# Performance work log

Hardware: AMD Instinct MI355X
Metric: run time of the kernel (lower is better)

## Reference

```python
import jax, jax.numpy as jnp
import numpy as np

HEADS = 8
DH = 160
LN_EPS = 1e-5


def _ln(x):
    m = jnp.mean(x, axis=-1, keepdims=True)
    v = jnp.var(x, axis=-1, keepdims=True)
    return (x - m) * jax.lax.rsqrt(v + LN_EPS)


def _adaln(x, table, w, b, t):
    # table[t]: [dim]; emb -> [2*dim]; chunk along dim 0 (scalar timestep)
    emb = jax.nn.silu(table[t]) @ w + b
    scale, shift = jnp.split(emb, 2)
    return _ln(x) * (1.0 + scale) + shift


def _attn(x, ctx, wq, wk, wv, wo, bo):
    B, S, _ = x.shape
    Sk = ctx.shape[1]
    q = (x @ wq).reshape(B, S, HEADS, DH).transpose(0, 2, 1, 3)    # [B,H,S,dh]
    k = (ctx @ wk).reshape(B, Sk, HEADS, DH).transpose(0, 2, 1, 3)
    v = (ctx @ wv).reshape(B, Sk, HEADS, DH).transpose(0, 2, 1, 3)
    scores = jnp.einsum('bhid,bhjd->bhij', q, k) * (DH ** -0.5)
    probs = jax.nn.softmax(scores, axis=-1)
    o = jnp.einsum('bhij,bhjd->bhid', probs, v)
    o = o.transpose(0, 2, 1, 3).reshape(B, S, HEADS * DH)
    return o @ wo + bo


def _ff(x, w1, b1, w2, b2):
    h, gate = jnp.split(x @ w1 + b1, 2, axis=-1)
    return (h * jax.nn.gelu(gate, approximate=False)) @ w2 + b2


def setup_inputs() -> dict:
    key = jax.random.key(0)
    ks = jax.random.split(key, 24)
    B, S, SC, DIM, CROSS, INNER = 2, 2048, 77, 1280, 768, 5120

    def w(k, shape, s=0.02):
        return jax.random.normal(k, shape, jnp.float32) * s

    return {
        'hidden_states': jax.random.normal(ks[0], (B, S, DIM), jnp.float32),
        'context': jax.random.normal(ks[1], (B, SC, CROSS), jnp.float32),
        'ada1_emb': w(ks[2], (1000, DIM)),
        'ada1_w': w(ks[3], (DIM, 2 * DIM)),
        'ada1_b': jnp.zeros((2 * DIM,), jnp.float32),
        'ada2_emb': w(ks[4], (1000, DIM)),
        'ada2_w': w(ks[5], (DIM, 2 * DIM)),
        'ada2_b': jnp.zeros((2 * DIM,), jnp.float32),
        'a1_wq': w(ks[6], (DIM, DIM)), 'a1_wk': w(ks[7], (DIM, DIM)),
        'a1_wv': w(ks[8], (DIM, DIM)), 'a1_wo': w(ks[9], (DIM, DIM)),
        'a1_bo': jnp.zeros((DIM,), jnp.float32),
        'a2_wq': w(ks[10], (DIM, DIM)), 'a2_wk': w(ks[11], (CROSS, DIM)),
        'a2_wv': w(ks[12], (CROSS, DIM)), 'a2_wo': w(ks[13], (DIM, DIM)),
        'a2_bo': jnp.zeros((DIM,), jnp.float32),
        'norm3_g': jnp.ones((DIM,), jnp.float32),
        'norm3_b': jnp.zeros((DIM,), jnp.float32),
        'ff_w1': w(ks[14], (DIM, 2 * INNER)),
        'ff_b1': jnp.zeros((2 * INNER,), jnp.float32),
        'ff_w2': w(ks[15], (INNER, DIM)),
        'ff_b2': jnp.zeros((DIM,), jnp.float32),
        'timestep': 500,
    }


def reference(hidden_states, context, ada1_emb, ada1_w, ada1_b, ada2_emb, ada2_w, ada2_b,
              a1_wq, a1_wk, a1_wv, a1_wo, a1_bo, a2_wq, a2_wk, a2_wv, a2_wo, a2_bo,
              norm3_g, norm3_b, ff_w1, ff_b1, ff_w2, ff_b2, timestep):
    x = hidden_states
    # self-attention with AdaLayerNorm
    h = _adaln(x, ada1_emb, ada1_w, ada1_b, timestep)
    x = x + _attn(h, h, a1_wq, a1_wk, a1_wv, a1_wo, a1_bo)
    # cross-attention with AdaLayerNorm
    h = _adaln(x, ada2_emb, ada2_w, ada2_b, timestep)
    x = x + _attn(h, context, a2_wq, a2_wk, a2_wv, a2_wo, a2_bo)
    # feed-forward with affine LayerNorm
    h = _ln(x) * norm3_g + norm3_b
    x = x + _ff(h, ff_w1, ff_b1, ff_w2, ff_b2)
    return x
```

## Files before the change

### kernel.cpp

```cpp
#include <hip/hip_runtime.h>

typedef __attribute__((ext_vector_type(8))) unsigned short ushort8;
typedef __attribute__((ext_vector_type(4))) float f32x4;
typedef __attribute__((ext_vector_type(8))) __bf16 bf16x8;
typedef unsigned short u16;

__device__ inline unsigned short f2bf(float f) {
  unsigned u = __float_as_uint(f);
  unsigned r = (u + 0x7fffu + ((u >> 16) & 1u)) >> 16;
  return (unsigned short)r;
}
__device__ inline float bf2f(unsigned short h) {
  return __uint_as_float(((unsigned)h) << 16);
}

__device__ __forceinline__ void gload_lds16(const void* g, void* l) {
  __builtin_amdgcn_global_load_lds(
      (const __attribute__((address_space(1))) void*)g,
      (__attribute__((address_space(3))) void*)l, 16, 0, 0);
}

__device__ __forceinline__ void decomp_bid(int nbx, int nby, int& z, int& bx, int& by) {
  int bid = blockIdx.x;
  const int nwg = gridDim.x;
  const int q8 = nwg >> 3, r8 = nwg & 7;
  const int xcd = bid & 7, i = bid >> 3;
  bid = (xcd < r8 ? xcd * (q8 + 1) : r8 * (q8 + 1) + (xcd - r8) * q8) + i;
  const int nbb = nbx * nby;
  z = bid / nbb;
  int rem = bid - z * nbb;
  if ((nby & 7) == 0) {
    const int chunk = nbx << 3;
    const int c = rem / chunk, w = rem - c * chunk;
    bx = w >> 3;
    by = (c << 3) + (w & 7);
  } else {
    by = rem / nbx;
    bx = rem - by * nbx;
  }
}

__global__ __launch_bounds__(512, 4) void gemm64(
    const u16* __restrict__ A, long lda, long sAo, long sAi,
    const u16* __restrict__ B, long ldb, long sBo, long sBi,
    void* __restrict__ C, long ldc, long sCo, long sCi,
    const float* __restrict__ bias, const float* __restrict__ resid, long ldr,
    int M, int N, int K, int nbx, int Hdiv, float alpha, int outF32)
{
  __shared__ __align__(128) char smem[65536];
  const int tid = threadIdx.x;
  const int lane = tid & 63, wave = tid >> 6;

  int z, bx, by;
  decomp_bid(nbx, M >> 7, z, bx, by);
  const int m0 = by << 7, n0 = bx << 7;
  const int zb = z / Hdiv, zh = z - zb * Hdiv;
  const u16* Ab = A + (long)zb * sAo + (long)zh * sAi;
  const u16* Bb = B + (long)zb * sBo + (long)zh * sBi;

  const int srow = tid >> 3;
  const int g8 = ((tid & 7) ^ (srow & 7)) * 8;
  long aoff[2], boff[2];
#pragma unroll
  for (int i = 0; i < 2; ++i) {
    aoff[i] = (long)(m0 + i * 64 + srow) * lda + g8;
    boff[i] = (long)(n0 + i * 64 + srow) * ldb + g8;
  }
  const int ldst = tid * 16;

  const int wm = (wave >> 2) * 64, wn = (wave & 3) * 32;
  const int r15 = lane & 15, kq = lane >> 4;
  const int offK0 = (kq ^ (lane & 7)) * 16;
  const int offK1 = ((4 + kq) ^ (lane & 7)) * 16;

  const int nt = K >> 6;

#define STAGE64(bufofs, k0)                                                       \
  do {                                                                            \
    _Pragma("unroll") for (int i = 0; i < 2; ++i)                                 \
        gload_lds16(Ab + aoff[i] + (k0), smem + (bufofs) + i * 8192 + ldst);      \
    _Pragma("unroll") for (int i = 0; i < 2; ++i)                                 \
        gload_lds16(Bb + boff[i] + (k0), smem + (bufofs) + 16384 + i * 8192 + ldst); \
  } while (0)

  STAGE64(0, 0);
  STAGE64(32768, 64);

  f32x4 acc[4][2] = {};

  for (int t = 0; t < nt; ++t) {
    const int cbuf = (t & 1) << 15;
    if (t < nt - 1) asm volatile("s_waitcnt vmcnt(4)" ::: "memory");
    else            asm volatile("s_waitcnt vmcnt(0)" ::: "memory");
    __builtin_amdgcn_s_barrier();

    bf16x8 bfr[2][2];
#pragma unroll
    for (int q = 0; q < 2; ++q) {
      if (q == 0) {
#pragma unroll
        for (int j = 0; j < 2; ++j) {
          const int bb = cbuf + 16384 + (wn + j * 16 + r15) * 128;
          bfr[j][0] = *(const bf16x8*)(smem + bb + offK0);
          bfr[j][1] = *(const bf16x8*)(smem + bb + offK1);
        }
      }
      bf16x8 af[2][2];
#pragma unroll
      for (int i2 = 0; i2 < 2; ++i2) {
        const int ab = cbuf + (wm + (q * 2 + i2) * 16 + r15) * 128;
        af[i2][0] = *(const bf16x8*)(smem + ab + offK0);
        af[i2][1] = *(const bf16x8*)(smem + ab + offK1);
      }
      __builtin_amdgcn_s_setprio(1);
#pragma unroll
      for (int kk = 0; kk < 2; ++kk)
#pragma unroll
        for (int i2 = 0; i2 < 2; ++i2)
#pragma unroll
          for (int j = 0; j < 2; ++j)
            acc[q * 2 + i2][j] = __builtin_amdgcn_mfma_f32_16x16x32_bf16(
                af[i2][kk], bfr[j][kk], acc[q * 2 + i2][j], 0, 0, 0);
      __builtin_amdgcn_s_setprio(0);
      __builtin_amdgcn_s_barrier();
    }
    if (t + 2 < nt) STAGE64(cbuf, (long)(t + 2) * 64);
  }
#undef STAGE64

  const long cbase = (long)zb * sCo + (long)zh * sCi;
  const int rb = (lane >> 4) * 4;
#pragma unroll
  for (int i = 0; i < 4; ++i) {
#pragma unroll
    for (int j = 0; j < 2; ++j) {
      const int gcol = n0 + wn + j * 16 + r15;
      if (gcol >= N) continue;
      const float bv = bias ? bias[gcol] : 0.f;
#pragma unroll
      for (int tt = 0; tt < 4; ++tt) {
        const int grow = m0 + wm + i * 16 + rb + tt;
        float val = acc[i][j][tt] * alpha + bv;
        if (resid) val += resid[(long)grow * ldr + gcol];
        const long cidx = cbase + (long)grow * ldc + gcol;
        if (outF32) ((float*)C)[cidx] = val;
        else ((u16*)C)[cidx] = f2bf(val);
      }
    }
  }
}

__global__ __launch_bounds__(512, 4) void gemm32(
    const u16* __restrict__ A, long lda, long sAo, long sAi,
    const u16* __restrict__ B, long ldb, long sBo, long sBi,
    void* __restrict__ C, long ldc, long sCo, long sCi,
    const float* __restrict__ bias, const float* __restrict__ resid, long ldr,
    int M, int N, int K, int nbx, int Hdiv, float alpha, int outF32)
{
  __shared__ __align__(128) char smem[32768];
  const int tid = threadIdx.x;
  const int lane = tid & 63, wave = tid >> 6;

  int z, bx, by;
  decomp_bid(nbx, M >> 7, z, bx, by);
  const int m0 = by << 7, n0 = bx << 7;
  const int zb = z / Hdiv, zh = z - zb * Hdiv;
  const u16* Ab = A + (long)zb * sAo + (long)zh * sAi;
  const u16* Bb = B + (long)zb * sBo + (long)zh * sBi;

  const int srow = tid >> 2;
  const int g8 = ((tid & 3) ^ ((tid >> 3) & 3)) * 8;
  const long aoff = (long)(m0 + srow) * lda + g8;
  const long boff = (long)(n0 + srow) * ldb + g8;
  const int ldst = tid * 16;

  const int wm = (wave >> 2) * 64, wn = (wave & 3) * 32;
  const int r15 = lane & 15, kq = lane >> 4;
  const int goff = (kq ^ ((r15 >> 1) & 3)) * 16;

  const int nt = K >> 5;

#define STAGE32(bufofs, k0)                                                \
  do {                                                                     \
    gload_lds16(Ab + aoff + (k0), smem + (bufofs) + ldst);                 \
    gload_lds16(Bb + boff + (k0), smem + (bufofs) + 8192 + ldst);          \
  } while (0)

  STAGE32(0, 0);
  STAGE32(16384, 32);

  f32x4 acc[4][2] = {};

  for (int t = 0; t < nt; ++t) {
    const int cbuf = (t & 1) << 14;
    if (t < nt - 1) asm volatile("s_waitcnt vmcnt(2)" ::: "memory");
    else            asm volatile("s_waitcnt vmcnt(0)" ::: "memory");
    __builtin_amdgcn_s_barrier();

    bf16x8 af[4], bfr[2];
#pragma unroll
    for (int i = 0; i < 4; ++i)
      af[i] = *(const bf16x8*)(smem + cbuf + (wm + i * 16 + r15) * 64 + goff);
#pragma unroll
    for (int j = 0; j < 2; ++j)
      bfr[j] = *(const bf16x8*)(smem + cbuf + 8192 + (wn + j * 16 + r15) * 64 + goff);

    __builtin_amdgcn_s_setprio(1);
#pragma unroll
    for (int i = 0; i < 4; ++i)
#pragma unroll
      for (int j = 0; j < 2; ++j)
        acc[i][j] = __builtin_amdgcn_mfma_f32_16x16x32_bf16(af[i], bfr[j], acc[i][j], 0, 0, 0);
    __builtin_amdgcn_s_setprio(0);
    __builtin_amdgcn_s_barrier();

    if (t + 2 < nt) STAGE32(cbuf, (long)(t + 2) * 32);
  }
#undef STAGE32

  const long cbase = (long)zb * sCo + (long)zh * sCi;
  const int rb = (lane >> 4) * 4;
#pragma unroll
  for (int i = 0; i < 4; ++i) {
#pragma unroll
    for (int j = 0; j < 2; ++j) {
      const int gcol = n0 + wn + j * 16 + r15;
      if (gcol >= N) continue;
      const float bv = bias ? bias[gcol] : 0.f;
#pragma unroll
      for (int tt = 0; tt < 4; ++tt) {
        const int grow = m0 + wm + i * 16 + rb + tt;
        float val = acc[i][j][tt] * alpha + bv;
        if (resid) val += resid[(long)grow * ldr + gcol];
        const long cidx = cbase + (long)grow * ldc + gcol;
        if (outF32) ((float*)C)[cidx] = val;
        else ((u16*)C)[cidx] = f2bf(val);
      }
    }
  }
}

__global__ __launch_bounds__(256) void gemm_nt(
    const u16* __restrict__ A, long lda, long sAo, long sAi,
    const u16* __restrict__ B, long ldb, long sBo, long sBi,
    void* __restrict__ C, long ldc, long sCo, long sCi,
    const float* __restrict__ bias,
    const float* __restrict__ resid, long ldr,
    int M, int N, int K, int Hdiv, float alpha, int outF32)
{
  __shared__ u16 As[128 * 32];
  __shared__ u16 Bs[128 * 32];
  const int tid = threadIdx.x;
  const int z = blockIdx.z;
  const int zb = z / Hdiv, zh = z % Hdiv;
  const u16* Ab = A + (long)zb * sAo + (long)zh * sAi;
  const u16* Bb = B + (long)zb * sBo + (long)zh * sBi;
  const long cbase = (long)zb * sCo + (long)zh * sCi;
  const int m0 = blockIdx.y * 128, n0 = blockIdx.x * 128;
  const int lane = tid & 63, wave = tid >> 6;
  const int wm = (wave >> 1) * 64, wn = (wave & 1) * 64;
  const int r15 = lane & 15, kb = (lane >> 4) * 8;

  f32x4 acc[4][4] = {};

  for (int k0 = 0; k0 < K; k0 += 32) {
#pragma unroll
    for (int it = 0; it < 2; ++it) {
      const int c = tid + it * 256;
      const int row = c >> 2, ko = (c & 3) * 8;
      ushort8 va = {0, 0, 0, 0, 0, 0, 0, 0};
      const int gm = m0 + row;
      if (gm < M) va = *reinterpret_cast<const ushort8*>(Ab + (long)gm * lda + k0 + ko);
      *reinterpret_cast<ushort8*>(&As[row * 32 + ko]) = va;
      ushort8 vb = {0, 0, 0, 0, 0, 0, 0, 0};
      const int gn = n0 + row;
      if (gn < N) vb = *reinterpret_cast<const ushort8*>(Bb + (long)gn * ldb + k0 + ko);
      *reinterpret_cast<ushort8*>(&Bs[row * 32 + ko]) = vb;
    }
    __syncthreads();
    bf16x8 af[4], bfr[4];
#pragma unroll
    for (int i = 0; i < 4; ++i)
      af[i] = *reinterpret_cast<const bf16x8*>(&As[(wm + i * 16 + r15) * 32 + kb]);
#pragma unroll
    for (int j = 0; j < 4; ++j)
      bfr[j] = *reinterpret_cast<const bf16x8*>(&Bs[(wn + j * 16 + r15) * 32 + kb]);
#pragma unroll
    for (int i = 0; i < 4; ++i)
#pragma unroll
      for (int j = 0; j < 4; ++j)
        acc[i][j] = __builtin_amdgcn_mfma_f32_16x16x32_bf16(af[i], bfr[j], acc[i][j], 0, 0, 0);
    __syncthreads();
  }

  const int rb = (lane >> 4) * 4;
#pragma unroll
  for (int i = 0; i < 4; ++i) {
#pragma unroll
    for (int j = 0; j < 4; ++j) {
      const int gcol = n0 + wn + j * 16 + r15;
      if (gcol >= N) continue;
#pragma unroll
      for (int t = 0; t < 4; ++t) {
        const int grow = m0 + wm + i * 16 + rb + t;
        if (grow >= M) continue;
        float val = acc[i][j][t] * alpha;
        if (bias) val += bias[gcol];
        if (resid) val += resid[(long)grow * ldr + gcol];
        const long cidx = cbase + (long)grow * ldc + gcol;
        if (outF32) ((float*)C)[cidx] = val;
        else ((u16*)C)[cidx] = f2bf(val);
      }
    }
  }
}

__global__ void transpose_convert(const float* __restrict__ in,
                                  u16* __restrict__ out, int R, int C) {
  __shared__ float tile[32][33];
  const int c0 = blockIdx.x * 32, r0 = blockIdx.y * 32;
  const int tx = threadIdx.x, ty = threadIdx.y;
  for (int i = ty; i < 32; i += 8) {
    const int r = r0 + i, c = c0 + tx;
    tile[i][tx] = (r < R && c < C) ? in[(long)r * C + c] : 0.f;
  }
  __syncthreads();
  for (int i = ty; i < 32; i += 8) {
    const int c = c0 + i, r = r0 + tx;
    if (c < C && r < R) out[(long)c * R + r] = f2bf(tile[tx][i]);
  }
}

__global__ void convert_bf16(const float* __restrict__ in,
                             u16* __restrict__ out, long n) {
  const long i = (long)blockIdx.x * 256 + threadIdx.x;
  if (i < n) out[i] = f2bf(in[i]);
}

__global__ __launch_bounds__(256) void adaln_emb(
    const float* __restrict__ t1, const float* __restrict__ w1, const float* __restrict__ b1,
    const float* __restrict__ t2, const float* __restrict__ w2, const float* __restrict__ b2,
    const int* __restrict__ tstep, float* __restrict__ e1, float* __restrict__ e2)
{
  const int which = blockIdx.y;
  const float* tb = which ? t2 : t1;
  const float* w = which ? w2 : w1;
  const float* bb = which ? b2 : b1;
  float* out = which ? e2 : e1;
  const int t = tstep[0];
  __shared__ float sil[1280];
  const int tid = threadIdx.x;
  for (int i = tid; i < 1280; i += 256) {
    const float xv = tb[(long)t * 1280 + i];
    sil[i] = xv / (1.f + expf(-xv));
  }
  __syncthreads();
  const int j = blockIdx.x * 256 + tid;
  float acc = bb[j];
  for (int k = 0; k < 1280; ++k) acc += sil[k] * w[(long)k * 2560 + j];
  out[j] = acc;
}

__global__ __launch_bounds__(256) void ln_mod(
    const float* __restrict__ x, u16* __restrict__ out,
    const float* __restrict__ emb, const float* __restrict__ g,
    const float* __restrict__ bv, int affine)
{
  const long row = blockIdx.x;
  const float* xr = x + row * 1280;
  const int tid = threadIdx.x;
  float v[5], s = 0.f, s2 = 0.f;
#pragma unroll
  for (int i = 0; i < 5; ++i) {
    const float t = xr[tid + i * 256];
    v[i] = t; s += t; s2 += t * t;
  }
  __shared__ float rs_[4], rs2_[4], bc[2];
  for (int off = 32; off; off >>= 1) {
    s += __shfl_down(s, off, 64);
    s2 += __shfl_down(s2, off, 64);
  }
  if ((tid & 63) == 0) { rs_[tid >> 6] = s; rs2_[tid >> 6] = s2; }
  __syncthreads();
  if (tid == 0) {
    const float S = rs_[0] + rs_[1] + rs_[2] + rs_[3];
    const float S2 = rs2_[0] + rs2_[1] + rs2_[2] + rs2_[3];
    const float mean = S * (1.f / 1280.f);
    const float var = S2 * (1.f / 1280.f) - mean * mean;
    bc[0] = mean; bc[1] = rsqrtf(var + 1e-5f);
  }
  __syncthreads();
  const float mean = bc[0], rstd = bc[1];
#pragma unroll
  for (int i = 0; i < 5; ++i) {
    const int c = tid + i * 256;
    const float ln = (v[i] - mean) * rstd;
    const float y = affine ? (ln * g[c] + bv[c]) : (ln * (1.f + emb[c]) + emb[1280 + c]);
    out[row * 1280 + c] = f2bf(y);
  }
}

__global__ void transpose_v_self(const u16* __restrict__ v, int ldv,
                                 u16* __restrict__ vt) {
  __shared__ u16 t[32][33];
  const int z = blockIdx.z, b = z >> 3, hh = z & 7;
  const int s0 = blockIdx.x * 32, d0 = blockIdx.y * 32;
  const int tx = threadIdx.x, ty = threadIdx.y;
  for (int i = ty; i < 32; i += 8) {
    const int d = d0 + tx;
    t[i][tx] = (d < 160) ? v[((long)(b * 2048 + s0 + i)) * ldv + hh * 160 + d]
                         : (u16)0;
  }
  __syncthreads();
  for (int i = ty; i < 32; i += 8) {
    const int d = d0 + i;
    if (d < 160) vt[((long)z * 160 + d) * 2048 + s0 + tx] = t[tx][i];
  }
}

__global__ void make_vct(const u16* __restrict__ vc,
                         u16* __restrict__ vct) {
  const int idx = blockIdx.x * 256 + threadIdx.x;
  if (idx >= 16 * 160 * 96) return;
  const int s = idx % 96;
  const int d = (idx / 96) % 160;
  const int z = idx / (96 * 160);
  const int b = z >> 3, hh = z & 7;
  u16 val = 0;
  if (s < 77) val = vc[((long)(b * 77 + s)) * 2560 + hh * 160 + d];
  vct[idx] = val;
}

__global__ __launch_bounds__(256) void softmax_self(u16* __restrict__ S) {
  const long row = blockIdx.x;
  u16* p = S + row * 2048;
  const int tid = threadIdx.x;
  const ushort8 raw = *reinterpret_cast<const ushort8*>(p + tid * 8);
  float v[8];
  float mx = -1e30f;
#pragma unroll
  for (int e = 0; e < 8; ++e) { v[e] = bf2f(raw[e]); mx = fmaxf(mx, v[e]); }
  __shared__ float red[8];
  for (int off = 32; off; off >>= 1) mx = fmaxf(mx, __shfl_down(mx, off, 64));
  if ((tid & 63) == 0) red[tid >> 6] = mx;
  __syncthreads();
  if (tid == 0) {
    float m = red[0];
    for (int w = 1; w < 4; ++w) m = fmaxf(m, red[w]);
    red[4] = m;
  }
  __syncthreads();
  mx = red[4];
  float s = 0.f;
#pragma unroll
  for (int e = 0; e < 8; ++e) { v[e] = expf(v[e] - mx); s += v[e]; }
  __syncthreads();
  for (int off = 32; off; off >>= 1) s += __shfl_down(s, off, 64);
  if ((tid & 63) == 0) red[tid >> 6] = s;
  __syncthreads();
  if (tid == 0) red[4] = red[0] + red[1] + red[2] + red[3];
  __syncthreads();
  const float inv = 1.f / red[4];
  ushort8 outv;
#pragma unroll
  for (int e = 0; e < 8; ++e) outv[e] = f2bf(v[e] * inv);
  *reinterpret_cast<ushort8*>(p + tid * 8) = outv;
}

__global__ __launch_bounds__(64) void softmax_cross(u16* __restrict__ S) {
  const long row = blockIdx.x;
  u16* p = S + row * 96;
  const int tid = threadIdx.x;
  const float v0 = (tid < 77) ? bf2f(p[tid]) : -1e30f;
  const float v1 = (tid + 64 < 77) ? bf2f(p[tid + 64]) : -1e30f;
  float mx = fmaxf(v0, v1);
  for (int off = 32; off; off >>= 1) mx = fmaxf(mx, __shfl_down(mx, off, 64));
  mx = __shfl(mx, 0, 64);
  const float e0 = (tid < 77) ? expf(v0 - mx) : 0.f;
  const float e1 = (tid + 64 < 77) ? expf(v1 - mx) : 0.f;
  float s = e0 + e1;
  for (int off = 32; off; off >>= 1) s += __shfl_down(s, off, 64);
  s = __shfl(s, 0, 64);
  const float inv = 1.f / s;
  p[tid] = (tid < 77) ? f2bf(e0 * inv) : (u16)0;
  if (tid + 64 < 96) p[tid + 64] = (tid + 64 < 77) ? f2bf(e1 * inv) : (u16)0;
}

__global__ __launch_bounds__(256) void geglu(const u16* __restrict__ ff1,
                                             u16* __restrict__ out) {
  const long gid = (long)blockIdx.x * 256 + threadIdx.x;
  if (gid >= (long)4096 * 640) return;
  const long i = gid / 640;
  const int jb = (int)(gid % 640) * 8;
  const ushort8 a = *reinterpret_cast<const ushort8*>(ff1 + i * 10240 + jb);
  const ushort8 gt = *reinterpret_cast<const ushort8*>(ff1 + i * 10240 + 5120 + jb);
  ushort8 o;
#pragma unroll
  for (int e = 0; e < 8; ++e) {
    const float av = bf2f(a[e]);
    const float gv = bf2f(gt[e]);
    const float gel = 0.5f * gv * (1.f + erff(gv * 0.7071067811865475f));
    o[e] = f2bf(av * gel);
  }
  *reinterpret_cast<ushort8*>(out + i * 5120 + jb) = o;
}

extern "C" void kernel_launch(void* const* d_in, const int* in_sizes, int n_in,
                              void* d_out, int out_size, void* d_ws, size_t ws_size,
                              hipStream_t stream) {
  (void)in_sizes; (void)n_in; (void)out_size; (void)ws_size;

  const float* hidden   = (const float*)d_in[0];
  const float* context  = (const float*)d_in[1];
  const float* ada1_tab = (const float*)d_in[2];
  const float* ada1_w   = (const float*)d_in[3];
  const float* ada1_b   = (const float*)d_in[4];
  const float* ada2_tab = (const float*)d_in[5];
  const float* ada2_w   = (const float*)d_in[6];
  const float* ada2_b   = (const float*)d_in[7];
  const float* a1_wq = (const float*)d_in[8];
  const float* a1_wk = (const float*)d_in[9];
  const float* a1_wv = (const float*)d_in[10];
  const float* a1_wo = (const float*)d_in[11];
  const float* a1_bo = (const float*)d_in[12];
  const float* a2_wq = (const float*)d_in[13];
  const float* a2_wk = (const float*)d_in[14];
  const float* a2_wv = (const float*)d_in[15];
  const float* a2_wo = (const float*)d_in[16];
  const float* a2_bo = (const float*)d_in[17];
  const float* n3_g  = (const float*)d_in[18];
  const float* n3_b  = (const float*)d_in[19];
  const float* ff_w1 = (const float*)d_in[20];
  const float* ff_b1 = (const float*)d_in[21];
  const float* ff_w2 = (const float*)d_in[22];
  const float* ff_b2 = (const float*)d_in[23];
  const int*   tstep = (const int*)d_in[24];
  float* xout = (float*)d_out;

  char* base = (char*)d_ws;
  size_t off = 0;
  auto alloc = [&](size_t bytes) -> void* {
    void* p = base + off;
    off = (off + bytes + 255) & ~(size_t)255;
    return p;
  };
  u16* wqkvT = (u16*)alloc((size_t)3 * 1280 * 1280 * 2);
  u16* wo1T = (u16*)alloc((size_t)1280 * 1280 * 2);
  u16* wq2T = (u16*)alloc((size_t)1280 * 1280 * 2);
  u16* wkv2T = (u16*)alloc((size_t)2 * 1280 * 768 * 2);
  u16* wo2T = (u16*)alloc((size_t)1280 * 1280 * 2);
  u16* w1T  = (u16*)alloc((size_t)10240 * 1280 * 2);
  u16* w2T  = (u16*)alloc((size_t)1280 * 5120 * 2);
  u16* ctxb = (u16*)alloc((size_t)154 * 768 * 2);
  float* emb1 = (float*)alloc(2560 * 4);
  float* emb2 = (float*)alloc(2560 * 4);
  u16* h   = (u16*)alloc((size_t)4096 * 1280 * 2);
  u16* qkv = (u16*)alloc((size_t)4096 * 3840 * 2);
  u16* vt  = (u16*)alloc((size_t)16 * 160 * 2048 * 2);
  u16* vct = (u16*)alloc((size_t)16 * 160 * 96 * 2);
  u16* o   = (u16*)alloc((size_t)4096 * 1280 * 2);
  u16* scores = (u16*)alloc((size_t)16 * 2048 * 2048 * 2);
  u16* qc = qkv;
  u16* kvc = o;
  u16* ffh = qkv;
  u16* ff1out = scores;

  auto g64 = [&](const u16* A, long lda, long sAo, long sAi,
                 const u16* B, long ldb, long sBo, long sBi,
                 void* C, long ldc, long sCo, long sCi,
                 const float* bias, const float* resid, long ldr,
                 int M, int N, int K, int batch, int Hdiv, float alpha, int outF32) {
    const int nbx = (N + 127) >> 7;
    const int nwg = nbx * (M >> 7) * batch;
    gemm64<<<nwg, 512, 0, stream>>>(A, lda, sAo, sAi, B, ldb, sBo, sBi,
                                    C, ldc, sCo, sCi, bias, resid, ldr,
                                    M, N, K, nbx, Hdiv, alpha, outF32);
  };
  auto g32 = [&](const u16* A, long lda, long sAo, long sAi,
                 const u16* B, long ldb, long sBo, long sBi,
                 void* C, long ldc, long sCo, long sCi,
                 const float* bias, const float* resid, long ldr,
                 int M, int N, int K, int batch, int Hdiv, float alpha, int outF32) {
    const int nbx = (N + 127) >> 7;
    const int nwg = nbx * (M >> 7) * batch;
    gemm32<<<nwg, 512, 0, stream>>>(A, lda, sAo, sAi, B, ldb, sBo, sBi,
                                    C, ldc, sCo, sCi, bias, resid, ldr,
                                    M, N, K, nbx, Hdiv, alpha, outF32);
  };
  auto gemm = [&](const u16* A, long lda, long sAo, long sAi,
                  const u16* B, long ldb, long sBo, long sBi,
                  void* C, long ldc, long sCo, long sCi,
                  const float* bias, const float* resid, long ldr,
                  int M, int N, int K, int batch, int Hdiv, float alpha, int outF32) {
    dim3 g((N + 127) / 128, (M + 127) / 128, batch);
    gemm_nt<<<g, 256, 0, stream>>>(A, lda, sAo, sAi, B, ldb, sBo, sBi, C, ldc, sCo, sCi,
                                   bias, resid, ldr, M, N, K, Hdiv, alpha, outF32);
  };
  auto tconv = [&](const float* in, u16* out, int R, int C) {
    transpose_convert<<<dim3((C + 31) / 32, (R + 31) / 32), dim3(32, 8), 0, stream>>>(in, out, R, C);
  };

  tconv(a1_wq, wqkvT, 1280, 1280);
  tconv(a1_wk, wqkvT + (size_t)1280 * 1280, 1280, 1280);
  tconv(a1_wv, wqkvT + (size_t)2 * 1280 * 1280, 1280, 1280);
  tconv(a1_wo, wo1T, 1280, 1280);
  tconv(a2_wq, wq2T, 1280, 1280);
  tconv(a2_wk, wkv2T, 768, 1280);
  tconv(a2_wv, wkv2T + (size_t)1280 * 768, 768, 1280);
  tconv(a2_wo, wo2T, 1280, 1280);
  tconv(ff_w1, w1T, 1280, 10240);
  tconv(ff_w2, w2T, 5120, 1280);
  {
    const long n = (long)154 * 768;
    convert_bf16<<<(int)((n + 255) / 256), 256, 0, stream>>>(context, ctxb, n);
  }
  adaln_emb<<<dim3(10, 2), 256, 0, stream>>>(ada1_tab, ada1_w, ada1_b,
                                             ada2_tab, ada2_w, ada2_b, tstep, emb1, emb2);

  const float ascale = 0.07905694150420949f;
  const long S2 = (long)2048 * 2048;
  u16* qs = qkv;
  u16* ks = qkv + 1280;
  u16* vs = qkv + 2560;

  ln_mod<<<4096, 256, 0, stream>>>(hidden, h, emb1, nullptr, nullptr, 0);
  g64(h, 1280, 0, 0, wqkvT, 1280, 0, 0, qkv, 3840, 0, 0,
      nullptr, nullptr, 0, 4096, 3840, 1280, 1, 1, 1.f, 0);
  transpose_v_self<<<dim3(64, 5, 16), dim3(32, 8), 0, stream>>>(vs, 3840, vt);
  g32(qs, 3840, (long)2048 * 3840, 160, ks, 3840, (long)2048 * 3840, 160,
      scores, 2048, 8 * S2, S2, nullptr, nullptr, 0,
      2048, 2048, 160, 16, 8, ascale, 0);
  softmax_self<<<16 * 2048, 256, 0, stream>>>(scores);
  g64(scores, 2048, 8 * S2, S2, vt, 2048, (long)8 * 160 * 2048, (long)160 * 2048,
      o, 1280, (long)2048 * 1280, 160, nullptr, nullptr, 0,
      2048, 160, 2048, 16, 8, 1.f, 0);
  g64(o, 1280, 0, 0, wo1T, 1280, 0, 0, xout, 1280, 0, 0,
      a1_bo, hidden, 1280, 4096, 1280, 1280, 1, 1, 1.f, 1);

  ln_mod<<<4096, 256, 0, stream>>>(xout, h, emb2, nullptr, nullptr, 0);
  g64(h, 1280, 0, 0, wq2T, 1280, 0, 0, qc, 1280, 0, 0,
      nullptr, nullptr, 0, 4096, 1280, 1280, 1, 1, 1.f, 0);
  gemm(ctxb, 768, 0, 0, wkv2T, 768, 0, 0, kvc, 2560, 0, 0, nullptr, nullptr, 0,
       154, 2560, 768, 1, 1, 1.f, 0);
  make_vct<<<(16 * 160 * 96 + 255) / 256, 256, 0, stream>>>(kvc + 1280, vct);
  g32(qc, 1280, (long)2048 * 1280, 160, kvc, 2560, (long)77 * 2560, 160,
      scores, 96, (long)8 * 2048 * 96, (long)2048 * 96, nullptr, nullptr, 0,
      2048, 77, 160, 16, 8, ascale, 0);
  softmax_cross<<<16 * 2048, 64, 0, stream>>>(scores);
  g32(scores, 96, (long)8 * 2048 * 96, (long)2048 * 96,
      vct, 96, (long)8 * 160 * 96, (long)160 * 96,
      o, 1280, (long)2048 * 1280, 160, nullptr, nullptr, 0,
      2048, 160, 96, 16, 8, 1.f, 0);
  g64(o, 1280, 0, 0, wo2T, 1280, 0, 0, xout, 1280, 0, 0,
      a2_bo, xout, 1280, 4096, 1280, 1280, 1, 1, 1.f, 1);

  ln_mod<<<4096, 256, 0, stream>>>(xout, h, nullptr, n3_g, n3_b, 1);
  g64(h, 1280, 0, 0, w1T, 1280, 0, 0, ff1out, 10240, 0, 0,
      ff_b1, nullptr, 0, 4096, 10240, 1280, 1, 1, 1.f, 0);
  geglu<<<(int)(((long)4096 * 640 + 255) / 256), 256, 0, stream>>>(ff1out, ffh);
  g64(ffh, 5120, 0, 0, w2T, 5120, 0, 0, xout, 1280, 0, 0,
      ff_b2, xout, 1280, 4096, 1280, 5120, 1, 1, 1.f, 1);
}
```

Baseline: 835.6 us.

## Add 256x256-tile 8-wave ping-pong GEMM for QKV and FF1 projections

Adds a new GEMM kernel with 256x256 output tiles, 128 KB of double-buffered LDS, and a phased schedule. Each phase interleaves the next tile's global-to-LDS loads with the MFMA work and uses barriers plus setprio to stagger the waves. The QKV projection (N=3840) and the FF1 projection (N=10240) switch to it. The aim is more data reuse per tile and better overlap of loads with compute on the two largest GEMMs. In exchange, the larger tile lowers occupancy and leaves fewer workgroups: 240 for QKV, fewer than the 256 CUs. The kernel also assumes M, N and K divide evenly by the tile sizes.

```diff
diff --git a/kernel.cpp b/kernel.cpp
--- a/kernel.cpp
+++ b/kernel.cpp
@@ -37,6 +37,127 @@
   } else {
     by = rem / nbx;
     bx = rem - by * nbx;
+  }
+}
+
+__global__ __launch_bounds__(512, 2) void gemm8p(
+    const u16* __restrict__ A, long lda, long sAo, long sAi,
+    const u16* __restrict__ B, long ldb, long sBo, long sBi,
+    void* __restrict__ C, long ldc, long sCo, long sCi,
+    const float* __restrict__ bias, const float* __restrict__ resid, long ldr,
+    int M, int N, int K, int nbx, int Hdiv, int outF32)
+{
+  __shared__ __align__(128) char smem[131072];
+  const int tid = threadIdx.x;
+  const int lane = tid & 63, wave = tid >> 6;
+  const int wr = wave >> 2, wc = wave & 3;
+
+  int z, bx, by;
+  decomp_bid(nbx, M >> 8, z, bx, by);
+  const int m0 = by << 8, n0 = bx << 8;
+  const int zb = z / Hdiv, zh = z - zb * Hdiv;
+  const u16* Ab = A + (long)zb * sAo + (long)zh * sAi;
+  const u16* Bb = B + (long)zb * sBo + (long)zh * sBi;
+
+  const int srow = tid >> 3;
+  const int g8 = ((tid & 7) ^ (srow & 7)) * 8;
+  const long aoff0 = (long)(m0 + srow) * lda + g8;
+  const long boff0 = (long)(n0 + srow) * ldb + g8;
+  const int ldst = tid * 16;
+
+  const int r15 = lane & 15, kq = lane >> 4;
+  const int offK0 = (kq ^ (lane & 7)) * 16;
+  const int offK1 = ((4 + kq) ^ (lane & 7)) * 16;
+  const int abase = wr * 16384;
+  const int bbase = 32768 + (wc >> 1) * 16384;
+  const int bcol = (wc & 1) * 64;
+
+  auto stgA = [&](int cb, int h, long kk) {
+    gload_lds16(Ab + aoff0 + (long)(h * 128) * lda + kk, smem + cb + h * 16384 + ldst);
+    gload_lds16(Ab + aoff0 + (long)(h * 128 + 64) * lda + kk, smem + cb + h * 16384 + 8192 + ldst);
+  };
+  auto stgB = [&](int cb, int h, long kk) {
+    gload_lds16(Bb + boff0 + (long)(h * 128) * ldb + kk, smem + cb + 32768 + h * 16384 + ldst);
+    gload_lds16(Bb + boff0 + (long)(h * 128 + 64) * ldb + kk, smem + cb + 32768 + h * 16384 + 8192 + ldst);
+  };
+
+  stgA(0, 0, 0); stgA(0, 1, 0); stgB(0, 0, 0); stgB(0, 1, 0);
+  stgB(65536, 0, 64); stgB(65536, 1, 64);
+  asm volatile("s_waitcnt vmcnt(4)" ::: "memory");
+  __builtin_amdgcn_s_barrier();
+
+  f32x4 acc[8][4] = {};
+  const int nIter = K >> 7;
+
+#define WVC(NL)                                                          \
+  do {                                                                   \
+    if (NL) asm volatile("s_waitcnt vmcnt(4)" ::: "memory");             \
+    else    asm volatile("s_waitcnt vmcnt(0)" ::: "memory");             \
+  } while (0)
+
+#define PHASE(CB, P, PREBAR, ...)                                        \
+  {                                                                      \
+    bf16x8 af[2][2];                                                     \
+    _Pragma("unroll") for (int i2 = 0; i2 < 2; ++i2) {                   \
+      const int ra = (CB) + abase + ((P) * 32 + i2 * 16 + r15) * 128;    \
+      af[i2][0] = *(const bf16x8*)(smem + ra + offK0);                   \
+      af[i2][1] = *(const bf16x8*)(smem + ra + offK1);                   \
+    }                                                                    \
+    if ((P) == 0) {                                                      \
+      _Pragma("unroll") for (int j = 0; j < 4; ++j) {                    \
+        const int rb2 = (CB) + bbase + (bcol + j * 16 + r15) * 128;      \
+        bfr[j][0] = *(const bf16x8*)(smem + rb2 + offK0);                \
+        bfr[j][1] = *(const bf16x8*)(smem + rb2 + offK1);                \
+      }                                                                  \
+    }                                                                    \
+    __VA_ARGS__;                                                         \
+    __builtin_amdgcn_s_barrier();                                        \
+    __builtin_amdgcn_s_setprio(1);                                       \
+    _Pragma("unroll") for (int kk = 0; kk < 2; ++kk)                     \
+      _Pragma("unroll") for (int i2 = 0; i2 < 2; ++i2)                   \
+        _Pragma("unroll") for (int j = 0; j < 4; ++j)                    \
+          acc[(P) * 2 + i2][j] = __builtin_amdgcn_mfma_f32_16x16x32_bf16(\
+              af[i2][kk], bfr[j][kk], acc[(P) * 2 + i2][j], 0, 0, 0);    \
+    __builtin_amdgcn_s_setprio(0);                                       \
+    PREBAR;                                                              \
+    __builtin_amdgcn_s_barrier();                                        \
+  }
+
+  for (int it = 0; it < nIter; ++it) {
+    const long k0 = (long)it << 7;
+    const bool nl = (it + 1 < nIter);
+    bf16x8 bfr[4][2];
+    PHASE(0, 0, (void)0, stgA(65536, 0, k0 + 64); stgA(65536, 1, k0 + 64))
+    PHASE(0, 1, (void)0, if (nl) stgB(0, 0, k0 + 128))
+    PHASE(0, 2, (void)0, if (nl) stgB(0, 1, k0 + 128))
+    PHASE(0, 3, WVC(nl), (void)0)
+    PHASE(65536, 0, (void)0, if (nl) stgA(0, 0, k0 + 128))
+    PHASE(65536, 1, (void)0, if (nl) stgA(0, 1, k0 + 128))
+    PHASE(65536, 2, (void)0, if (nl) stgB(65536, 0, k0 + 192))
+    PHASE(65536, 3, WVC(nl), if (nl) stgB(65536, 1, k0 + 192))
+  }
+#undef PHASE
+#undef WVC
+
+  const long cbase = (long)zb * sCo + (long)zh * sCi;
+  const int rb = (lane >> 4) * 4;
+#pragma unroll
+  for (int i = 0; i < 8; ++i) {
+#pragma unroll
+    for (int j = 0; j < 4; ++j) {
+      const int gcol = n0 + wc * 64 + j * 16 + r15;
+      if (gcol >= N) continue;
+      const float bv = bias ? bias[gcol] : 0.f;
+#pragma unroll
+      for (int tt = 0; tt < 4; ++tt) {
+        const int grow = m0 + wr * 128 + i * 16 + rb + tt;
+        float val = acc[i][j][tt] + bv;
+        if (resid) val += resid[(long)grow * ldr + gcol];
+        const long cidx = cbase + (long)grow * ldc + gcol;
+        if (outF32) ((float*)C)[cidx] = val;
+        else ((u16*)C)[cidx] = f2bf(val);
+      }
+    }
   }
 }
 
@@ -565,6 +686,15 @@
   u16* ffh = qkv;
   u16* ff1out = scores;
 
+  auto g8p = [&](const u16* A, long lda, const u16* B, long ldb,
+                 void* C, long ldc, const float* bias, const float* resid, long ldr,
+                 int M, int N, int K, int outF32) {
+    const int nbx = N >> 8;
+    const int nwg = nbx * (M >> 8);
+    gemm8p<<<nwg, 512, 0, stream>>>(A, lda, 0, 0, B, ldb, 0, 0,
+                                    C, ldc, 0, 0, bias, resid, ldr,
+                                    M, N, K, nbx, 1, outF32);
+  };
   auto g64 = [&](const u16* A, long lda, long sAo, long sAi,
                  const u16* B, long ldb, long sBo, long sBi,
                  void* C, long ldc, long sCo, long sCi,
@@ -624,8 +754,7 @@
   u16* vs = qkv + 2560;
 
   ln_mod<<<4096, 256, 0, stream>>>(hidden, h, emb1, nullptr, nullptr, 0);
-  g64(h, 1280, 0, 0, wqkvT, 1280, 0, 0, qkv, 3840, 0, 0,
-      nullptr, nullptr, 0, 4096, 3840, 1280, 1, 1, 1.f, 0);
+  g8p(h, 1280, wqkvT, 1280, qkv, 3840, nullptr, nullptr, 0, 4096, 3840, 1280, 0);
   transpose_v_self<<<dim3(64, 5, 16), dim3(32, 8), 0, stream>>>(vs, 3840, vt);
   g32(qs, 3840, (long)2048 * 3840, 160, ks, 3840, (long)2048 * 3840, 160,
       scores, 2048, 8 * S2, S2, nullptr, nullptr, 0,
@@ -655,8 +784,7 @@
       a2_bo, xout, 1280, 4096, 1280, 1280, 1, 1, 1.f, 1);
 
   ln_mod<<<4096, 256, 0, stream>>>(xout, h, nullptr, n3_g, n3_b, 1);
-  g64(h, 1280, 0, 0, w1T, 1280, 0, 0, ff1out, 10240, 0, 0,
-      ff_b1, nullptr, 0, 4096, 10240, 1280, 1, 1, 1.f, 0);
+  g8p(h, 1280, w1T, 1280, ff1out, 10240, ff_b1, nullptr, 0, 4096, 10240, 1280, 0);
   geglu<<<(int)(((long)4096 * 640 + 255) / 256), 256, 0, stream>>>(ff1out, ffh);
   g64(ffh, 5120, 0, 0, w2T, 5120, 0, 0, xout, 1280, 0, 0,
       ff_b2, xout, 1280, 4096, 1280, 5120, 1, 1, 1.f, 1);
```

Result: slower. 853.5 us (+2.2%).

## Fuse self-attention QK^T, softmax and PV into a flash-attention kernel

Applied to the files above, without the earlier changes.

Replaces the three-step self-attention (score GEMM into a bf16 score buffer, row softmax kernel, PV GEMM) with one flash-style kernel. It uses an online softmax over 64-key tiles, double-buffers K/V through registers into LDS, and uses MFMA 16x16x32 bf16. This removes the write and re-read of the 16x2048x2048 score matrix and two launches. In exchange it runs only 256 workgroups of 512 threads, each iterating sequentially over all keys, and it shrinks the score buffer while giving the FF intermediate its own allocation.

```diff
diff --git a/kernel.cpp b/kernel.cpp
--- a/kernel.cpp
+++ b/kernel.cpp
@@ -38,6 +38,165 @@
     by = rem / nbx;
     bx = rem - by * nbx;
   }
+}
+
+__global__ __launch_bounds__(512, 2) void flash_self(
+    const u16* __restrict__ qkv, const u16* __restrict__ vtg, u16* __restrict__ o)
+{
+  __shared__ __align__(128) u16 Qs[128 * 168];
+  __shared__ __align__(128) u16 Ks[2][64 * 168];
+  __shared__ __align__(128) u16 Vs[2][160 * 64];
+  __shared__ __align__(128) u16 Ps[128 * 64];
+
+  const int tid = threadIdx.x;
+  const int lane = tid & 63, wave = tid >> 6;
+  const int r15 = lane & 15, kq = lane >> 4;
+  const int z = blockIdx.x >> 4, qt = blockIdx.x & 15;
+  const int b = z >> 3, hh = z & 7;
+  const u16* Qg = qkv + ((long)(b * 2048 + qt * 128)) * 3840 + hh * 160;
+  const u16* Kg = qkv + ((long)(b * 2048)) * 3840 + 1280 + hh * 160;
+  const u16* Vg = vtg + (long)z * 160 * 2048;
+
+  for (int c = tid; c < 2560; c += 512) {
+    const int r = c / 20, e = (c % 20) * 8;
+    *(ushort8*)&Qs[r * 168 + e] = *(const ushort8*)(Qg + (long)r * 3840 + e);
+  }
+  const int c0 = tid, c1 = tid + 512, c2 = tid + 1024;
+  const bool has2 = (c2 < 1280);
+  const int kR0 = c0 / 20, kE0 = (c0 % 20) * 8;
+  const int kR1 = c1 / 20, kE1 = (c1 % 20) * 8;
+  const int kR2 = has2 ? c2 / 20 : 0, kE2 = has2 ? (c2 % 20) * 8 : 0;
+  const int vR0 = c0 >> 3, vG0 = c0 & 7;
+  const int vR1 = c1 >> 3, vG1 = c1 & 7;
+  const int vR2 = has2 ? (c2 >> 3) : 0, vG2 = has2 ? (c2 & 7) : 0;
+
+  {
+    ushort8 k0 = *(const ushort8*)(Kg + (long)kR0 * 3840 + kE0);
+    ushort8 k1 = *(const ushort8*)(Kg + (long)kR1 * 3840 + kE1);
+    ushort8 v0 = *(const ushort8*)(Vg + (long)vR0 * 2048 + vG0 * 8);
+    ushort8 v1 = *(const ushort8*)(Vg + (long)vR1 * 2048 + vG1 * 8);
+    *(ushort8*)&Ks[0][kR0 * 168 + kE0] = k0;
+    *(ushort8*)&Ks[0][kR1 * 168 + kE1] = k1;
+    *(ushort8*)&Vs[0][vR0 * 64 + ((vG0 ^ (vR0 & 7)) * 8)] = v0;
+    *(ushort8*)&Vs[0][vR1 * 64 + ((vG1 ^ (vR1 & 7)) * 8)] = v1;
+    if (has2) {
+      ushort8 k2 = *(const ushort8*)(Kg + (long)kR2 * 3840 + kE2);
+      ushort8 v2 = *(const ushort8*)(Vg + (long)vR2 * 2048 + vG2 * 8);
+      *(ushort8*)&Ks[0][kR2 * 168 + kE2] = k2;
+      *(ushort8*)&Vs[0][vR2 * 64 + ((vG2 ^ (vR2 & 7)) * 8)] = v2;
+    }
+  }
+  __syncthreads();
+
+  bf16x8 qf[5];
+#pragma unroll
+  for (int kf = 0; kf < 5; ++kf)
+    qf[kf] = *(const bf16x8*)&Qs[(wave * 16 + r15) * 168 + kf * 32 + kq * 8];
+
+  float m[4], l[4] = {0.f, 0.f, 0.f, 0.f};
+#pragma unroll
+  for (int t = 0; t < 4; ++t) m[t] = -1e30f;
+  f32x4 accO[10] = {};
+  const float SC = 0.07905694150420949f;
+
+  ushort8 kr0, kr1, kr2, vr0, vr1, vr2;
+
+  for (int step = 0; step < 32; ++step) {
+    const int cur = step & 1;
+    const bool nl = step < 31;
+    if (nl) {
+      const long kv1 = (long)(step + 1) * 64;
+      kr0 = *(const ushort8*)(Kg + (kv1 + kR0) * 3840 + kE0);
+      kr1 = *(const ushort8*)(Kg + (kv1 + kR1) * 3840 + kE1);
+      vr0 = *(const ushort8*)(Vg + (long)vR0 * 2048 + kv1 + vG0 * 8);
+      vr1 = *(const ushort8*)(Vg + (long)vR1 * 2048 + kv1 + vG1 * 8);
+      if (has2) {
+        kr2 = *(const ushort8*)(Kg + (kv1 + kR2) * 3840 + kE2);
+        vr2 = *(const ushort8*)(Vg + (long)vR2 * 2048 + kv1 + vG2 * 8);
+      }
+    }
+    f32x4 sa[4] = {};
+#pragma unroll
+    for (int nf = 0; nf < 4; ++nf)
+#pragma unroll
+      for (int kf = 0; kf < 5; ++kf) {
+        const bf16x8 kfrag =
+            *(const bf16x8*)&Ks[cur][(nf * 16 + r15) * 168 + kf * 32 + kq * 8];
+        sa[nf] = __builtin_amdgcn_mfma_f32_16x16x32_bf16(qf[kf], kfrag, sa[nf], 0, 0, 0);
+      }
+    float corr[4];
+#pragma unroll
+    for (int t = 0; t < 4; ++t) {
+      float tm = fmaxf(fmaxf(sa[0][t], sa[1][t]), fmaxf(sa[2][t], sa[3][t])) * SC;
+      tm = fmaxf(tm, __shfl_xor(tm, 1, 64));
+      tm = fmaxf(tm, __shfl_xor(tm, 2, 64));
+      tm = fmaxf(tm, __shfl_xor(tm, 4, 64));
+      tm = fmaxf(tm, __shfl_xor(tm, 8, 64));
+      const float mn = fmaxf(m[t], tm);
+      corr[t] = __expf(m[t] - mn);
+      m[t] = mn;
+    }
+    const int qr0 = wave * 16 + kq * 4;
+#pragma unroll
+    for (int t = 0; t < 4; ++t) {
+      float rs = 0.f;
+      const int qr = qr0 + t;
+#pragma unroll
+      for (int nf = 0; nf < 4; ++nf) {
+        const float p = __expf(sa[nf][t] * SC - m[t]);
+        rs += p;
+        const int col = r15 + nf * 16;
+        Ps[qr * 64 + (((col >> 3) ^ (qr & 7)) * 8) + (col & 7)] = f2bf(p);
+      }
+      rs += __shfl_xor(rs, 1, 64);
+      rs += __shfl_xor(rs, 2, 64);
+      rs += __shfl_xor(rs, 4, 64);
+      rs += __shfl_xor(rs, 8, 64);
+      l[t] = l[t] * corr[t] + rs;
+    }
+#pragma unroll
+    for (int j = 0; j < 10; ++j)
+#pragma unroll
+      for (int t = 0; t < 4; ++t) accO[j][t] *= corr[t];
+    if (nl) {
+      const int nxt = cur ^ 1;
+      *(ushort8*)&Ks[nxt][kR0 * 168 + kE0] = kr0;
+      *(ushort8*)&Ks[nxt][kR1 * 168 + kE1] = kr1;
+      *(ushort8*)&Vs[nxt][vR0 * 64 + ((vG0 ^ (vR0 & 7)) * 8)] = vr0;
+      *(ushort8*)&Vs[nxt][vR1 * 64 + ((vG1 ^ (vR1 & 7)) * 8)] = vr1;
+      if (has2) {
+        *(ushort8*)&Ks[nxt][kR2 * 168 + kE2] = kr2;
+        *(ushort8*)&Vs[nxt][vR2 * 64 + ((vG2 ^ (vR2 & 7)) * 8)] = vr2;
+      }
+    }
+    __syncthreads();
+    const int arow = wave * 16 + r15;
+    bf16x8 pf[2];
+#pragma unroll
+    for (int k2 = 0; k2 < 2; ++k2)
+      pf[k2] = *(const bf16x8*)&Ps[arow * 64 + (((k2 * 4 + kq) ^ (arow & 7)) * 8)];
+#pragma unroll
+    for (int j = 0; j < 10; ++j)
+#pragma unroll
+      for (int k2 = 0; k2 < 2; ++k2) {
+        const int vrow = j * 16 + r15;
+        const bf16x8 vf =
+            *(const bf16x8*)&Vs[cur][vrow * 64 + (((k2 * 4 + kq) ^ (vrow & 7)) * 8)];
+        accO[j] = __builtin_amdgcn_mfma_f32_16x16x32_bf16(pf[k2], vf, accO[j], 0, 0, 0);
+      }
+    __syncthreads();
+  }
+  float inv[4];
+#pragma unroll
+  for (int t = 0; t < 4; ++t) inv[t] = 1.f / l[t];
+  u16* orow = o + ((long)(b * 2048 + qt * 128)) * 1280 + hh * 160;
+#pragma unroll
+  for (int j = 0; j < 10; ++j)
+#pragma unroll
+    for (int t = 0; t < 4; ++t) {
+      const int qr = wave * 16 + kq * 4 + t;
+      orow[(long)qr * 1280 + j * 16 + r15] = f2bf(accO[j][t] * inv[t]);
+    }
 }
 
 __global__ __launch_bounds__(512, 4) void gemm64(
@@ -429,42 +588,6 @@
   u16 val = 0;
   if (s < 77) val = vc[((long)(b * 77 + s)) * 2560 + hh * 160 + d];
   vct[idx] = val;
-}
-
-__global__ __launch_bounds__(256) void softmax_self(u16* __restrict__ S) {
-  const long row = blockIdx.x;
-  u16* p = S + row * 2048;
-  const int tid = threadIdx.x;
-  const ushort8 raw = *reinterpret_cast<const ushort8*>(p + tid * 8);
-  float v[8];
-  float mx = -1e30f;
-#pragma unroll
-  for (int e = 0; e < 8; ++e) { v[e] = bf2f(raw[e]); mx = fmaxf(mx, v[e]); }
-  __shared__ float red[8];
-  for (int off = 32; off; off >>= 1) mx = fmaxf(mx, __shfl_down(mx, off, 64));
-  if ((tid & 63) == 0) red[tid >> 6] = mx;
-  __syncthreads();
-  if (tid == 0) {
-    float m = red[0];
-    for (int w = 1; w < 4; ++w) m = fmaxf(m, red[w]);
-    red[4] = m;
-  }
-  __syncthreads();
-  mx = red[4];
-  float s = 0.f;
-#pragma unroll
-  for (int e = 0; e < 8; ++e) { v[e] = expf(v[e] - mx); s += v[e]; }
-  __syncthreads();
-  for (int off = 32; off; off >>= 1) s += __shfl_down(s, off, 64);
-  if ((tid & 63) == 0) red[tid >> 6] = s;
-  __syncthreads();
-  if (tid == 0) red[4] = red[0] + red[1] + red[2] + red[3];
-  __syncthreads();
-  const float inv = 1.f / red[4];
-  ushort8 outv;
-#pragma unroll
-  for (int e = 0; e < 8; ++e) outv[e] = f2bf(v[e] * inv);
-  *reinterpret_cast<ushort8*>(p + tid * 8) = outv;
 }
 
 __global__ __launch_bounds__(64) void softmax_cross(u16* __restrict__ S) {
@@ -559,11 +682,11 @@
   u16* vt  = (u16*)alloc((size_t)16 * 160 * 2048 * 2);
   u16* vct = (u16*)alloc((size_t)16 * 160 * 96 * 2);
   u16* o   = (u16*)alloc((size_t)4096 * 1280 * 2);
-  u16* scores = (u16*)alloc((size_t)16 * 2048 * 2048 * 2);
+  u16* scores = (u16*)alloc((size_t)16 * 2048 * 96 * 2);
   u16* qc = qkv;
   u16* kvc = o;
   u16* ffh = qkv;
-  u16* ff1out = scores;
+  u16* ff1out = (u16*)alloc((size_t)4096 * 10240 * 2);
 
   auto g64 = [&](const u16* A, long lda, long sAo, long sAi,
                  const u16* B, long ldb, long sBo, long sBi,
@@ -618,32 +741,24 @@
                                              ada2_tab, ada2_w, ada2_b, tstep, emb1, emb2);
 
   const float ascale = 0.07905694150420949f;
-  const long S2 = (long)2048 * 2048;
-  u16* qs = qkv;
-  u16* ks = qkv + 1280;
+  u16* qc_ = qc;
   u16* vs = qkv + 2560;
 
   ln_mod<<<4096, 256, 0, stream>>>(hidden, h, emb1, nullptr, nullptr, 0);
   g64(h, 1280, 0, 0, wqkvT, 1280, 0, 0, qkv, 3840, 0, 0,
       nullptr, nullptr, 0, 4096, 3840, 1280, 1, 1, 1.f, 0);
   transpose_v_self<<<dim3(64, 5, 16), dim3(32, 8), 0, stream>>>(vs, 3840, vt);
-  g32(qs, 3840, (long)2048 * 3840, 160, ks, 3840, (long)2048 * 3840, 160,
-      scores, 2048, 8 * S2, S2, nullptr, nullptr, 0,
-      2048, 2048, 160, 16, 8, ascale, 0);
-  softmax_self<<<16 * 2048, 256, 0, stream>>>(scores);
-  g64(scores, 2048, 8 * S2, S2, vt, 2048, (long)8 * 160 * 2048, (long)160 * 2048,
-      o, 1280, (long)2048 * 1280, 160, nullptr, nullptr, 0,
-      2048, 160, 2048, 16, 8, 1.f, 0);
+  flash_self<<<256, 512, 0, stream>>>(qkv, vt, o);
   g64(o, 1280, 0, 0, wo1T, 1280, 0, 0, xout, 1280, 0, 0,
       a1_bo, hidden, 1280, 4096, 1280, 1280, 1, 1, 1.f, 1);
 
   ln_mod<<<4096, 256, 0, stream>>>(xout, h, emb2, nullptr, nullptr, 0);
-  g64(h, 1280, 0, 0, wq2T, 1280, 0, 0, qc, 1280, 0, 0,
+  g64(h, 1280, 0, 0, wq2T, 1280, 0, 0, qc_, 1280, 0, 0,
       nullptr, nullptr, 0, 4096, 1280, 1280, 1, 1, 1.f, 0);
   gemm(ctxb, 768, 0, 0, wkv2T, 768, 0, 0, kvc, 2560, 0, 0, nullptr, nullptr, 0,
        154, 2560, 768, 1, 1, 1.f, 0);
   make_vct<<<(16 * 160 * 96 + 255) / 256, 256, 0, stream>>>(kvc + 1280, vct);
-  g32(qc, 1280, (long)2048 * 1280, 160, kvc, 2560, (long)77 * 2560, 160,
+  g32(qc_, 1280, (long)2048 * 1280, 160, kvc, 2560, (long)77 * 2560, 160,
       scores, 96, (long)8 * 2048 * 96, (long)2048 * 96, nullptr, nullptr, 0,
       2048, 77, 160, 16, 8, ascale, 0);
   softmax_cross<<<16 * 2048, 64, 0, stream>>>(scores);
```

Result: faster. 718.8 us (-14.0%).
